# Kernel optimization log

Hardware: AMD Instinct MI355X
Metric: run time of the kernel (lower is better)

Reference implementation:

```python
import jax, jax.numpy as jnp
import numpy as np

DEPTH = 4
DIM = 768
HEADS = 12
DH = 64
INNER = HEADS * DH            # 768
FF_INNER = int(4 * (2.0 / 3.0) * DIM)  # 2048 (GEGLU paper sizing)
B, N = 4, 1024                # N must be a perfect square (2D rotary)
ATTN_SCALE = 8.0              # cosine-sim attention scale from Attention(scale=8)
EPS = 1e-5


def _ln(x, gamma, beta):
    mu = jnp.mean(x, axis=-1, keepdims=True)
    var = jnp.mean((x - mu) ** 2, axis=-1, keepdims=True)
    return (x - mu) * jax.lax.rsqrt(var + EPS) * gamma + beta


def _rope_angles(n, dh):
    # precompute_freqs_cis_2d: x/y positions on sqrt(n) grid, dh//4 freqs each, interleaved
    H = int(n ** 0.5)
    pos = jnp.arange(n)
    xp = (pos % H).astype(jnp.float32)
    yp = (pos // H).astype(jnp.float32)
    freqs = 1.0 / (10000.0 ** (jnp.arange(0, dh, 4)[: dh // 4].astype(jnp.float32) / dh))
    xa = jnp.outer(xp, freqs)  # [n, dh//4]
    ya = jnp.outer(yp, freqs)
    return jnp.stack([xa, ya], axis=-1).reshape(n, dh // 2)  # [n, dh//2]


def _apply_rope(t, cos, sin):
    # t: [B, N, H, DH]; complex-pair rotation on last dim
    tr = t.reshape(*t.shape[:-1], DH // 2, 2)
    r, im = tr[..., 0], tr[..., 1]
    c = cos[None, :, None, :]
    s = sin[None, :, None, :]
    out = jnp.stack([r * c - im * s, r * s + im * c], axis=-1)
    return out.reshape(t.shape)


def _l2norm(t):
    return t / jnp.maximum(jnp.linalg.norm(t, axis=-1, keepdims=True), 1e-12)


def setup_inputs() -> dict:
    key = jax.random.key(0)
    ks = jax.random.split(key, 10)
    w = 0.02
    return {
        "x": jax.random.normal(ks[0], (B, N, DIM), dtype=jnp.float32),
        "attn_gamma": jnp.ones((DEPTH, DIM), dtype=jnp.float32),
        "wq": w * jax.random.normal(ks[1], (DEPTH, DIM, INNER), dtype=jnp.float32),
        "wkv": w * jax.random.normal(ks[2], (DEPTH, DIM, 2 * INNER), dtype=jnp.float32),
        "q_scale": jnp.ones((DEPTH, DH), dtype=jnp.float32),
        "k_scale": jnp.ones((DEPTH, DH), dtype=jnp.float32),
        "wo": w * jax.random.normal(ks[3], (DEPTH, INNER, DIM), dtype=jnp.float32),
        "ff_gamma": jnp.ones((DEPTH, DIM), dtype=jnp.float32),
        "ff_beta": jnp.zeros((DEPTH, DIM), dtype=jnp.float32),
        "wff1": w * jax.random.normal(ks[4], (DEPTH, DIM, 2 * FF_INNER), dtype=jnp.float32),
        "wff2": w * jax.random.normal(ks[5], (DEPTH, FF_INNER, DIM), dtype=jnp.float32),
    }


def reference(x, attn_gamma, wq, wkv, q_scale, k_scale, wo, ff_gamma, ff_beta, wff1, wff2):
    b, n, _ = x.shape
    ang = _rope_angles(n, DH)
    cos, sin = jnp.cos(ang), jnp.sin(ang)
    for i in range(DEPTH):
        # ---- Attention (qk-l2norm cosine attention, 2D rotary, scale=8) ----
        h = _ln(x, attn_gamma[i], 0.0)          # Attention.norm (beta is a zero buffer)
        kv_in = x                                # faithful: kv_input taken BEFORE norm
        q = (h @ wq[i]).reshape(b, n, HEADS, DH)
        kv = kv_in @ wkv[i]
        k, v = jnp.split(kv, 2, axis=-1)
        k = k.reshape(b, n, HEADS, DH)
        v = v.reshape(b, n, HEADS, DH)
        q = _apply_rope(q, cos, sin)
        k = _apply_rope(k, cos, sin)
        q = jnp.transpose(q, (0, 2, 1, 3))       # b h n d
        k = jnp.transpose(k, (0, 2, 1, 3))
        v = jnp.transpose(v, (0, 2, 1, 3))
        q = _l2norm(q) * q_scale[i]
        k = _l2norm(k) * k_scale[i]
        sim = jnp.einsum('bhid,bhjd->bhij', q, k) * ATTN_SCALE
        attn = jax.nn.softmax(sim, axis=-1)
        o = jnp.einsum('bhij,bhjd->bhid', attn, v)
        o = jnp.transpose(o, (0, 2, 1, 3)).reshape(b, n, INNER)
        x = x + o @ wo[i]
        # ---- GEGLU FeedForward ----
        hf = _ln(x, ff_gamma[i], ff_beta[i])
        u = hf @ wff1[i]
        a, g = jnp.split(u, 2, axis=-1)
        x = x + (a * jax.nn.gelu(g, approximate=False)) @ wff2[i]
    return x
```

## Files before the change

### kernel.cpp

```cpp
#include <hip/hip_runtime.h>
#include <hip/hip_bf16.h>
#include <math.h>

typedef __hip_bfloat16 bf16;
typedef __bf16 bf16x8 __attribute__((ext_vector_type(8)));
typedef float f32x4 __attribute__((ext_vector_type(4)));

#define NDEPTH 4
#define DIM 768
#define HEADS 12
#define DH 64
#define INNER 768
#define FFI 2048
#define BB 4
#define NN 1024
#define ROWS (BB*NN)

__device__ __forceinline__ void async_cp16(const bf16* g, bf16* l) {
  __builtin_amdgcn_global_load_lds(
      (const __attribute__((address_space(1))) unsigned int*)g,
      (__attribute__((address_space(3))) unsigned int*)l, 16, 0, 0);
}

template<int BN, bool GELU, bool VOUT, int K, int LD>
__device__ __forceinline__ void gemm_body(
    const bf16* __restrict__ A, const bf16* __restrict__ Bt,
    bf16* __restrict__ Cb, float* __restrict__ Cf, const float* __restrict__ Rf,
    bf16* __restrict__ Vt, int M, int N, int bx, int by, bf16* As, bf16* Bs)
{
  constexpr int WN = BN / 2;
  constexpr int NT = WN / 16;
  const int tid  = threadIdx.x;
  const int lane = tid & 63, w = tid >> 6;
  const int quad = lane >> 4, l16 = lane & 15;
  const int wr = w >> 1, wc = w & 1;
  const int m0 = by * 128, n0 = bx * BN;

  f32x4 acc[4][NT] = {};

  constexpr int CHA = 128 * 8;
  constexpr int CH  = CHA + BN * 8;
  constexpr int NCH = CH / 256;
  constexpr int NTK = K / 64;

  auto stage = [&](int kk, int buf) {
    bf16* Asb = As + buf * (128*64);
    bf16* Bsb = Bs + buf * (BN*64);
    #pragma unroll
    for (int t = 0; t < NCH; ++t) {
      int c0 = w*64 + t*256;
      int ch = c0 + lane;
      if (c0 < CHA) {
        int r = ch >> 3, j = (ch & 7) ^ (r & 7);
        async_cp16(&A[(size_t)(m0 + r)*LD + kk + j*8], &Asb[(size_t)c0*8]);
      } else {
        int ch2 = ch - CHA, r = ch2 >> 3, j = (ch2 & 7) ^ (r & 7);
        async_cp16(&Bt[(size_t)(n0 + r)*LD + kk + j*8], &Bsb[(size_t)(c0 - CHA)*8]);
      }
    }
  };

  stage(0, 0);
  __syncthreads();

  #pragma unroll
  for (int t = 0; t < NTK; ++t) {
    const int buf = t & 1;
    if (t + 1 < NTK) stage((t + 1) * 64, buf ^ 1);

    const bf16* Asb = As + buf * (128*64);
    const bf16* Bsb = Bs + buf * (BN*64);

    #pragma unroll
    for (int kc = 0; kc < 2; ++kc) {
      bf16x8 bfr[NT];
      #pragma unroll
      for (int nt = 0; nt < NT; ++nt) {
        int rb = wc*WN + nt*16 + l16;
        int c  = (kc*4 + quad) ^ (rb & 7);
        bfr[nt] = *(const bf16x8*)&Bsb[rb*64 + c*8];
      }
      #pragma unroll
      for (int mt = 0; mt < 4; ++mt) {
        int ra = wr*64 + mt*16 + l16;
        int ca = (kc*4 + quad) ^ (ra & 7);
        bf16x8 af = *(const bf16x8*)&Asb[ra*64 + ca*8];
        #pragma unroll
        for (int nt = 0; nt < NT; ++nt)
          acc[mt][nt] = __builtin_amdgcn_mfma_f32_16x16x32_bf16(af, bfr[nt], acc[mt][nt], 0, 0, 0);
      }
    }
    if (t + 1 < NTK) __syncthreads();
  }

  #pragma unroll
  for (int mt = 0; mt < 4; ++mt) {
    #pragma unroll
    for (int nt = 0; nt < NT; ++nt) {
      int row = m0 + wr*64 + mt*16 + quad*4;
      int col = n0 + wc*WN + nt*16 + l16;
      if (GELU) {
        #pragma unroll
        for (int r = 0; r < 4; ++r) {
          float v = acc[mt][nt][r];
          float g = __shfl_xor(v, 1);
          if (!(lane & 1)) {
            float ge = 0.5f * g * (1.f + erff(g * 0.70710678118654752f));
            Cb[(size_t)(row + r)*(N >> 1) + (col >> 1)] = __float2bfloat16(v * ge);
          }
        }
      } else if (VOUT) {
        if (col < INNER) {
          #pragma unroll
          for (int r = 0; r < 4; ++r)
            Cb[(size_t)(row + r)*INNER + col] = __float2bfloat16(acc[mt][nt][r]);
        } else {
          int c2 = col - INNER, hh = c2 >> 6, d = c2 & 63;
          int b = row >> 10, nn = row & 1023;
          union { ushort4 u4; bf16 h4[4]; } p;
          #pragma unroll
          for (int r = 0; r < 4; ++r) p.h4[r] = __float2bfloat16(acc[mt][nt][r]);
          *(ushort4*)&Vt[(((size_t)b*HEADS + hh)*DH + d)*NN + nn] = p.u4;
        }
      } else {
        #pragma unroll
        for (int r = 0; r < 4; ++r) {
          float v = acc[mt][nt][r];
          size_t idx = (size_t)(row + r) * N + col;
          if (Rf) v += Rf[idx];
          if (Cf) Cf[idx] = v;
          if (Cb) Cb[idx] = __float2bfloat16(v);
        }
      }
    }
  }
}

template<int BN, int KH, int LD>
__global__ __launch_bounds__(256) void gemm_splitk_kernel(
    const bf16* __restrict__ A, const bf16* __restrict__ Bt,
    float* __restrict__ P, int M, int N)
{
  __shared__ __align__(16) bf16 As[2*128*64];
  __shared__ __align__(16) bf16 Bs[2*BN*64];
  const int z = blockIdx.z;
  gemm_body<BN,false,false,KH,LD>(A + (size_t)z*KH, Bt + (size_t)z*KH, nullptr,
                                  P + (size_t)z*M*N, nullptr, nullptr,
                                  M, N, blockIdx.x, blockIdx.y, As, Bs);
}

__global__ __launch_bounds__(256) void qkv_kernel(
    const bf16* __restrict__ h, const bf16* __restrict__ x16,
    const bf16* __restrict__ wqT, const bf16* __restrict__ wkvT,
    bf16* __restrict__ qb, bf16* __restrict__ kb, bf16* __restrict__ vt)
{
  __shared__ __align__(16) bf16 As[2*128*64];
  __shared__ __align__(16) bf16 Bs[2*128*64];
  if (blockIdx.z == 0)
    gemm_body<64,false,false,768,768>(h, wqT, qb, nullptr, nullptr, nullptr,
                                      ROWS, INNER, blockIdx.x, blockIdx.y, As, Bs);
  else
    gemm_body<128,false,true,768,768>(x16, wkvT, kb, nullptr, nullptr, vt,
                                      ROWS, 2*INNER, blockIdx.x, blockIdx.y, As, Bs);
}

__global__ __launch_bounds__(512) void gemm256_kernel(
    const bf16* __restrict__ A, const bf16* __restrict__ Bt,
    bf16* __restrict__ Cb, int M, int N)
{
  __shared__ __align__(16) bf16 As[2][256*64];
  __shared__ __align__(16) bf16 Bs[2][256*64];

  const int tid  = threadIdx.x;
  const int lane = tid & 63, wv = tid >> 6;
  const int quad = lane >> 4, l16 = lane & 15;
  const int wr = wv >> 2, wc = wv & 3;
  const int m0 = blockIdx.y * 256, n0 = blockIdx.x * 256;

  f32x4 acc[8][4] = {};

  auto stage = [&](int kk, int buf) {
    #pragma unroll
    for (int t = 0; t < 8; ++t) {
      int c0 = wv*64 + t*512;
      int ch = c0 + lane;
      if (c0 < 2048) {
        int r = ch >> 3, j = (ch & 7) ^ (r & 7);
        async_cp16(&A[(size_t)(m0 + r)*768 + kk + j*8], &As[buf][(size_t)c0*8]);
      } else {
        int ch2 = ch - 2048, r = ch2 >> 3, j = (ch2 & 7) ^ (r & 7);
        async_cp16(&Bt[(size_t)(n0 + r)*768 + kk + j*8], &Bs[buf][(size_t)(c0 - 2048)*8]);
      }
    }
  };

  stage(0, 0);
  __syncthreads();

  #pragma unroll
  for (int t = 0; t < 12; ++t) {
    const int buf = t & 1;
    if (t + 1 < 12) stage((t + 1) * 64, buf ^ 1);

    const bf16* Asb = &As[buf][0];
    const bf16* Bsb = &Bs[buf][0];

    #pragma unroll
    for (int kc = 0; kc < 2; ++kc) {
      bf16x8 bfr[4];
      #pragma unroll
      for (int nt = 0; nt < 4; ++nt) {
        int rb = wc*64 + nt*16 + l16;
        int c  = (kc*4 + quad) ^ (rb & 7);
        bfr[nt] = *(const bf16x8*)&Bsb[rb*64 + c*8];
      }
      #pragma unroll
      for (int mt = 0; mt < 8; ++mt) {
        int ra = wr*128 + mt*16 + l16;
        int ca = (kc*4 + quad) ^ (ra & 7);
        bf16x8 af = *(const bf16x8*)&Asb[ra*64 + ca*8];
        #pragma unroll
        for (int nt = 0; nt < 4; ++nt)
          acc[mt][nt] = __builtin_amdgcn_mfma_f32_16x16x32_bf16(af, bfr[nt], acc[mt][nt], 0, 0, 0);
      }
    }
    if (t + 1 < 12) __syncthreads();
  }

  #pragma unroll
  for (int mt = 0; mt < 8; ++mt) {
    #pragma unroll
    for (int nt = 0; nt < 4; ++nt) {
      int row = m0 + wr*128 + mt*16 + quad*4;
      int col = n0 + wc*64 + nt*16 + l16;
      #pragma unroll
      for (int r = 0; r < 4; ++r) {
        float v = acc[mt][nt][r];
        float g = __shfl_xor(v, 1);
        if (!(lane & 1)) {
          float ge = 0.5f * g * (1.f + erff(g * 0.70710678118654752f));
          Cb[(size_t)(row + r)*(N >> 1) + (col >> 1)] = __float2bfloat16(v * ge);
        }
      }
    }
  }
}

__global__ __launch_bounds__(256) void ln_kernel(
    const float* __restrict__ x, const float* __restrict__ g,
    const float* __restrict__ bta, bf16* __restrict__ out)
{
  const int row = blockIdx.x, tid = threadIdx.x;
  const size_t base = (size_t)row * DIM;
  float v[3];
  #pragma unroll
  for (int j = 0; j < 3; ++j) v[j] = x[base + tid + j*256];
  float s  = v[0] + v[1] + v[2];
  float ss = v[0]*v[0] + v[1]*v[1] + v[2]*v[2];
  #pragma unroll
  for (int off = 32; off; off >>= 1) { s += __shfl_xor(s, off); ss += __shfl_xor(ss, off); }
  __shared__ float red[8];
  int w = tid >> 6;
  if ((tid & 63) == 0) { red[w] = s; red[w + 4] = ss; }
  __syncthreads();
  s  = red[0] + red[1] + red[2] + red[3];
  ss = red[4] + red[5] + red[6] + red[7];
  float mean = s * (1.f/768.f);
  float var  = ss * (1.f/768.f) - mean*mean;
  float rstd = rsqrtf(fmaxf(var, 0.f) + 1e-5f);
  #pragma unroll
  for (int j = 0; j < 3; ++j) {
    int c = tid + j*256;
    float bv = bta ? bta[c] : 0.f;
    out[base + c] = __float2bfloat16((v[j] - mean) * rstd * g[c] + bv);
  }
}

__global__ __launch_bounds__(256) void redln_kernel(
    const float* __restrict__ P0, const float* __restrict__ P1,
    const float* __restrict__ res,
    float* __restrict__ xo32, bf16* __restrict__ xo16, float* __restrict__ outf,
    const float* __restrict__ g, const float* __restrict__ bta,
    bf16* __restrict__ lnout)
{
  const int row = blockIdx.x, tid = threadIdx.x;
  const size_t base = (size_t)row * DIM;
  float v[3];
  #pragma unroll
  for (int j = 0; j < 3; ++j) {
    size_t idx = base + tid + j*256;
    v[j] = res[idx] + P0[idx] + P1[idx];
    if (xo32) xo32[idx] = v[j];
    if (xo16) xo16[idx] = __float2bfloat16(v[j]);
    if (outf) outf[idx] = v[j];
  }
  if (!g) return;
  float s  = v[0] + v[1] + v[2];
  float ss = v[0]*v[0] + v[1]*v[1] + v[2]*v[2];
  #pragma unroll
  for (int off = 32; off; off >>= 1) { s += __shfl_xor(s, off); ss += __shfl_xor(ss, off); }
  __shared__ float red[8];
  int w = tid >> 6;
  if ((tid & 63) == 0) { red[w] = s; red[w + 4] = ss; }
  __syncthreads();
  s  = red[0] + red[1] + red[2] + red[3];
  ss = red[4] + red[5] + red[6] + red[7];
  float mean = s * (1.f/768.f);
  float var  = ss * (1.f/768.f) - mean*mean;
  float rstd = rsqrtf(fmaxf(var, 0.f) + 1e-5f);
  #pragma unroll
  for (int j = 0; j < 3; ++j) {
    int c = tid + j*256;
    float bv = bta ? bta[c] : 0.f;
    lnout[base + c] = __float2bfloat16((v[j] - mean) * rstd * g[c] + bv);
  }
}

__global__ __launch_bounds__(384) void rope_kernel(
    const bf16* __restrict__ q, const bf16* __restrict__ kb,
    const float* __restrict__ qsc, const float* __restrict__ ksc,
    bf16* __restrict__ qh, bf16* __restrict__ kh)
{
  const int bn = blockIdx.x;
  const int b = bn >> 10, n = bn & 1023;
  const int tid = threadIdx.x;
  const int h = tid >> 5, pr = tid & 31, d0 = pr*2;
  const float xp = (float)(n & 31), yp = (float)(n >> 5);
  const int t = pr >> 1;
  const float freq = powf(10000.f, -(float)t / 16.f);
  const float ang = (pr & 1) ? yp * freq : xp * freq;
  float sn, cs;
  sincosf(ang, &sn, &cs);
  const float2 qs2 = *(const float2*)&qsc[d0];
  const float2 ks2 = *(const float2*)&ksc[d0];

  union { unsigned int u; bf16 h2[2]; } qa, ka, qo, ko;
  qa.u = *(const unsigned int*)&q [(size_t)bn*INNER + h*64 + d0];
  ka.u = *(const unsigned int*)&kb[(size_t)bn*INNER + h*64 + d0];
  float qre = __bfloat162float(qa.h2[0]), qim = __bfloat162float(qa.h2[1]);
  float kre = __bfloat162float(ka.h2[0]), kim = __bfloat162float(ka.h2[1]);
  float qr = qre*cs - qim*sn, qi = qre*sn + qim*cs;
  float kr = kre*cs - kim*sn, ki = kre*sn + kim*cs;
  float q2 = qr*qr + qi*qi, k2 = kr*kr + ki*ki;
  #pragma unroll
  for (int off = 1; off < 32; off <<= 1) { q2 += __shfl_xor(q2, off); k2 += __shfl_xor(k2, off); }
  float qinv = 8.f / fmaxf(sqrtf(q2), 1e-12f);
  float kinv = 1.f / fmaxf(sqrtf(k2), 1e-12f);
  qo.h2[0] = __float2bfloat16(qr * qinv * qs2.x);
  qo.h2[1] = __float2bfloat16(qi * qinv * qs2.y);
  ko.h2[0] = __float2bfloat16(kr * kinv * ks2.x);
  ko.h2[1] = __float2bfloat16(ki * kinv * ks2.y);
  size_t oi = (((size_t)b*HEADS + h)*NN + n)*DH + d0;
  *(unsigned int*)&qh[oi] = qo.u;
  *(unsigned int*)&kh[oi] = ko.u;
}

__global__ __launch_bounds__(256) void attn_kernel(
    const bf16* __restrict__ qh, const bf16* __restrict__ kh,
    const bf16* __restrict__ vt, const float* __restrict__ qsc,
    const float* __restrict__ ksc, bf16* __restrict__ ob)
{
  __shared__ __align__(16) bf16 Qs[64*72];
  __shared__ __align__(16) bf16 Ks[64*72];
  __shared__ __align__(16) bf16 Vt[64*72];
  __shared__ __align__(16) bf16 Ps[4][16*72];

  const int tid = threadIdx.x;
  const int lane = tid & 63, w = tid >> 6;
  const int quad = lane >> 4, l16 = lane & 15;
  const int qt = blockIdx.x, bh = blockIdx.y;
  const int b = bh / HEADS, h = bh % HEADS;
  const size_t base = (size_t)bh * NN * DH;

  float mq = fabsf(qsc[lane]), mk = fabsf(ksc[lane]);
  #pragma unroll
  for (int off = 1; off < 64; off <<= 1) {
    mq = fmaxf(mq, __shfl_xor(mq, off));
    mk = fmaxf(mk, __shfl_xor(mk, off));
  }
  const float Mb = 8.f * mq * mk;

  for (int c = tid; c < 512; c += 256) {
    int r = c >> 3, j = c & 7;
    *(uint4*)&Qs[r*72 + j*8] = *(const uint4*)&qh[base + (size_t)(qt*64 + r)*64 + j*8];
  }

  f32x4 o[4] = {};
  float pl[4] = {0.f, 0.f, 0.f, 0.f};

  for (int kt0 = 0; kt0 < NN/64; ++kt0) {
    __syncthreads();
    for (int c = tid; c < 512; c += 256) {
      int r = c >> 3, j = c & 7;
      *(uint4*)&Ks[r*72 + j*8] = *(const uint4*)&kh[base + (size_t)(kt0*64 + r)*64 + j*8];
      *(uint4*)&Vt[r*72 + j*8] = *(const uint4*)&vt[base + (size_t)r*NN + kt0*64 + j*8];
    }
    __syncthreads();

    f32x4 s[4] = {};
    bf16x8 aq[2];
    #pragma unroll
    for (int kc = 0; kc < 2; ++kc)
      aq[kc] = *(const bf16x8*)&Qs[(w*16 + l16)*72 + kc*32 + quad*8];
    #pragma unroll
    for (int kt = 0; kt < 4; ++kt)
      #pragma unroll
      for (int kc = 0; kc < 2; ++kc) {
        bf16x8 bk = *(const bf16x8*)&Ks[(kt*16 + l16)*72 + kc*32 + quad*8];
        s[kt] = __builtin_amdgcn_mfma_f32_16x16x32_bf16(aq[kc], bk, s[kt], 0, 0, 0);
      }

    #pragma unroll
    for (int r = 0; r < 4; ++r) {
      #pragma unroll
      for (int kt = 0; kt < 4; ++kt) {
        float pv = __expf(s[kt][r] - Mb);
        pl[r] += pv;
        Ps[w][(quad*4 + r)*72 + kt*16 + l16] = __float2bfloat16(pv);
      }
    }

    #pragma unroll
    for (int kc = 0; kc < 2; ++kc) {
      bf16x8 ap = *(const bf16x8*)&Ps[w][l16*72 + kc*32 + quad*8];
      #pragma unroll
      for (int nt = 0; nt < 4; ++nt) {
        bf16x8 bv = *(const bf16x8*)&Vt[(nt*16 + l16)*72 + kc*32 + quad*8];
        o[nt] = __builtin_amdgcn_mfma_f32_16x16x32_bf16(ap, bv, o[nt], 0, 0, 0);
      }
    }
  }

  float l[4];
  #pragma unroll
  for (int r = 0; r < 4; ++r) {
    float rs = pl[r];
    #pragma unroll
    for (int off = 1; off < 16; off <<= 1) rs += __shfl_xor(rs, off);
    l[r] = rs;
  }

  #pragma unroll
  for (int nt = 0; nt < 4; ++nt)
    #pragma unroll
    for (int r = 0; r < 4; ++r) {
      int n = qt*64 + w*16 + quad*4 + r;
      int dcol = nt*16 + l16;
      ob[((size_t)(b*NN + n)*HEADS + h)*DH + dcol] = __float2bfloat16(o[nt][r] / l[r]);
    }
}

__global__ __launch_bounds__(256) void cast_kernel(
    const float* __restrict__ x, bf16* __restrict__ o)
{
  size_t i = ((size_t)blockIdx.x*256 + threadIdx.x) * 8;
  float4 f0 = *(const float4*)(x + i);
  float4 f1 = *(const float4*)(x + i + 4);
  union { uint4 u; bf16 h[8]; } p;
  p.h[0] = __float2bfloat16(f0.x); p.h[1] = __float2bfloat16(f0.y);
  p.h[2] = __float2bfloat16(f0.z); p.h[3] = __float2bfloat16(f0.w);
  p.h[4] = __float2bfloat16(f1.x); p.h[5] = __float2bfloat16(f1.y);
  p.h[6] = __float2bfloat16(f1.z); p.h[7] = __float2bfloat16(f1.w);
  *(uint4*)(o + i) = p.u;
}

struct TD { const float* src; bf16* dst; int R, C, base, perm; };
struct TDs5 { TD d[5]; };

__global__ __launch_bounds__(256) void wtrans_kernel(TDs5 a)
{
  const int blk = blockIdx.x;
  int di = 0;
  #pragma unroll
  for (int k = 1; k < 5; ++k) if (blk >= a.d[k].base) di = k;
  const TD d = a.d[di];
  const int local = blk - d.base;
  const int tilesX = d.C >> 5;
  const int by = local / tilesX, bx = local - by*tilesX;
  __shared__ float t[32][33];
  const int tx = threadIdx.x & 31, ty = threadIdx.x >> 5;
  const int c0 = bx*32, r0 = by*32;
  #pragma unroll
  for (int i = 0; i < 4; ++i)
    t[ty + i*8][tx] = d.src[(size_t)(r0 + ty + i*8)*d.C + c0 + tx];
  __syncthreads();
  const int half = d.C >> 1;
  #pragma unroll
  for (int i = 0; i < 4; ++i) {
    int c = c0 + ty + i*8;
    int rout = d.perm ? ((c < half) ? 2*c : 2*(c - half) + 1) : c;
    d.dst[(size_t)rout*d.R + r0 + tx] = __float2bfloat16(t[tx][ty + i*8]);
  }
}

extern "C" void kernel_launch(void* const* d_in, const int* in_sizes, int n_in,
                              void* d_out, int out_size, void* d_ws, size_t ws_size,
                              hipStream_t stream)
{
  const float* x_in       = (const float*)d_in[0];
  const float* attn_gamma = (const float*)d_in[1];
  const float* wq         = (const float*)d_in[2];
  const float* wkv        = (const float*)d_in[3];
  const float* q_scale    = (const float*)d_in[4];
  const float* k_scale    = (const float*)d_in[5];
  const float* wo         = (const float*)d_in[6];
  const float* ff_gamma   = (const float*)d_in[7];
  const float* ff_beta    = (const float*)d_in[8];
  const float* wff1       = (const float*)d_in[9];
  const float* wff2       = (const float*)d_in[10];
  float* outp = (float*)d_out;
  char* ws = (char*)d_ws;

  const size_t E = (size_t)ROWS * DIM;
  float* xw32 = (float*)ws;
  bf16*  xw16 = (bf16*)(ws + 12582912);
  bf16*  S_h  = (bf16*)(ws + 18874368);
  char*  BIGb = ws + 25165824;
  bf16*  WT   = (bf16*)(ws + 62914560);
  bf16*  qbuf  = (bf16*)BIGb;
  bf16*  kbuf  = qbuf + E;
  bf16*  qhb   = qbuf + 2*E;
  bf16*  khb   = qbuf + 3*E;
  bf16*  vtb   = qbuf + 4*E;
  bf16*  glbuf = (bf16*)BIGb;
  float* wP    = (float*)BIGb;
  float* fP    = (float*)(BIGb + 16777216);
  bf16*  wqT   = WT;
  bf16*  wkvT  = WT + 589824;
  bf16*  woT   = WT + 1769472;
  bf16*  wff1T = WT + 2359296;
  bf16*  wff2T = WT + 5505024;

  cast_kernel<<<1536, 256, 0, stream>>>(x_in, xw16);
  ln_kernel<<<ROWS, 256, 0, stream>>>(x_in, attn_gamma, nullptr, S_h);

  for (int i = 0; i < NDEPTH; ++i) {
    const float* xsrc = (i == 0) ? x_in : xw32;

    TDs5 td;
    td.d[0] = { wq   + (size_t)i*589824,  wqT,   768,  768,    0, 0 };
    td.d[1] = { wkv  + (size_t)i*1179648, wkvT,  768, 1536,  576, 0 };
    td.d[2] = { wo   + (size_t)i*589824,  woT,   768,  768, 1728, 0 };
    td.d[3] = { wff1 + (size_t)i*3145728, wff1T, 768, 4096, 2304, 1 };
    td.d[4] = { wff2 + (size_t)i*1572864, wff2T, 2048, 768, 5376, 0 };
    wtrans_kernel<<<6912, 256, 0, stream>>>(td);

    qkv_kernel<<<dim3(12,32,2), 256, 0, stream>>>(S_h, xw16, wqT, wkvT, qbuf, kbuf, vtb);
    rope_kernel<<<ROWS, 384, 0, stream>>>(qbuf, kbuf, q_scale + i*DH, k_scale + i*DH, qhb, khb);
    attn_kernel<<<dim3(16,48), 256, 0, stream>>>(qhb, khb, vtb,
                                                 q_scale + i*DH, k_scale + i*DH, S_h);
    gemm_splitk_kernel<64,384,768><<<dim3(12,32,2), 256, 0, stream>>>(S_h, woT, wP, ROWS, DIM);
    redln_kernel<<<ROWS, 256, 0, stream>>>(wP, wP + E, xsrc, xw32, nullptr, nullptr,
                                           ff_gamma + i*DIM, ff_beta + i*DIM, S_h);
    gemm256_kernel<<<dim3(16,16), 512, 0, stream>>>(S_h, wff1T, glbuf, ROWS, 2*FFI);
    gemm_splitk_kernel<64,1024,2048><<<dim3(12,32,2), 256, 0, stream>>>(glbuf, wff2T, fP, ROWS, DIM);
    if (i < NDEPTH-1)
      redln_kernel<<<ROWS, 256, 0, stream>>>(fP, fP + E, xw32, xw32, xw16, nullptr,
                                             attn_gamma + (i+1)*DIM, nullptr, S_h);
    else
      redln_kernel<<<ROWS, 256, 0, stream>>>(fP, fP + E, xw32, nullptr, nullptr, outp,
                                             nullptr, nullptr, nullptr);
  }
}
```

Baseline: 936.8 us.

## Double-buffer attention K/V tiles with async LDS loads and remap GEMM256 blocks per XCD

The attention kernel now loads Q, K and V with asynchronous global-to-LDS copies into XOR-swizzled, unpadded shared-memory tiles. K/V are double-buffered so the next tile's load overlaps the current tile's MFMA and softmax work, and one barrier per iteration is removed. Separately, the 256x256 GEMM remaps its linear block index so that blocks landing on the same XCD cover neighbouring tiles, to improve L2 reuse. The remap hardcodes a 16x16 grid shape, and the async loads rely on the barrier to wait for outstanding copies.

```diff
diff --git a/kernel.cpp b/kernel.cpp
--- a/kernel.cpp
+++ b/kernel.cpp
@@ -175,7 +175,12 @@
   const int lane = tid & 63, wv = tid >> 6;
   const int quad = lane >> 4, l16 = lane & 15;
   const int wr = wv >> 2, wc = wv & 3;
-  const int m0 = blockIdx.y * 256, n0 = blockIdx.x * 256;
+
+  const int lin = blockIdx.y * gridDim.x + blockIdx.x;
+  const int xcd = lin & 7, loc = lin >> 3;
+  const int bxs = (xcd & 1) * 8 + (loc & 7);
+  const int bys = (xcd >> 1) * 4 + (loc >> 3);
+  const int m0 = bys * 256, n0 = bxs * 256;
 
   f32x4 acc[8][4] = {};
 
@@ -360,9 +365,9 @@
     const bf16* __restrict__ vt, const float* __restrict__ qsc,
     const float* __restrict__ ksc, bf16* __restrict__ ob)
 {
-  __shared__ __align__(16) bf16 Qs[64*72];
-  __shared__ __align__(16) bf16 Ks[64*72];
-  __shared__ __align__(16) bf16 Vt[64*72];
+  __shared__ __align__(16) bf16 Qs[64*64];
+  __shared__ __align__(16) bf16 Ks[2][64*64];
+  __shared__ __align__(16) bf16 Vs[2][64*64];
   __shared__ __align__(16) bf16 Ps[4][16*72];
 
   const int tid = threadIdx.x;
@@ -380,33 +385,51 @@
   }
   const float Mb = 8.f * mq * mk;
 
-  for (int c = tid; c < 512; c += 256) {
-    int r = c >> 3, j = c & 7;
-    *(uint4*)&Qs[r*72 + j*8] = *(const uint4*)&qh[base + (size_t)(qt*64 + r)*64 + j*8];
-  }
+  #pragma unroll
+  for (int t = 0; t < 2; ++t) {
+    int c0 = w*64 + t*256, ch = c0 + lane;
+    int r = ch >> 3, jl = (ch & 7) ^ (r & 7);
+    async_cp16(&qh[base + (size_t)(qt*64 + r)*64 + jl*8], &Qs[(size_t)c0*8]);
+  }
+
+  auto stage_kv = [&](int kt0, int buf) {
+    #pragma unroll
+    for (int t = 0; t < 4; ++t) {
+      int c0 = w*64 + t*256, ch = c0 + lane;
+      if (c0 < 512) {
+        int r = ch >> 3, jl = (ch & 7) ^ (r & 7);
+        async_cp16(&kh[base + (size_t)(kt0*64 + r)*64 + jl*8],
+                   &Ks[buf][(size_t)c0*8]);
+      } else {
+        int ch2 = ch - 512, r = ch2 >> 3, jl = (ch2 & 7) ^ (r & 7);
+        async_cp16(&vt[base + (size_t)r*NN + kt0*64 + jl*8],
+                   &Vs[buf][(size_t)(c0 - 512)*8]);
+      }
+    }
+  };
 
   f32x4 o[4] = {};
   float pl[4] = {0.f, 0.f, 0.f, 0.f};
 
+  stage_kv(0, 0);
+  __syncthreads();
+
   for (int kt0 = 0; kt0 < NN/64; ++kt0) {
-    __syncthreads();
-    for (int c = tid; c < 512; c += 256) {
-      int r = c >> 3, j = c & 7;
-      *(uint4*)&Ks[r*72 + j*8] = *(const uint4*)&kh[base + (size_t)(kt0*64 + r)*64 + j*8];
-      *(uint4*)&Vt[r*72 + j*8] = *(const uint4*)&vt[base + (size_t)r*NN + kt0*64 + j*8];
-    }
-    __syncthreads();
+    const int buf = kt0 & 1;
+    if (kt0 + 1 < NN/64) stage_kv(kt0 + 1, buf ^ 1);
 
     f32x4 s[4] = {};
     bf16x8 aq[2];
+    const int rq = w*16 + l16;
     #pragma unroll
     for (int kc = 0; kc < 2; ++kc)
-      aq[kc] = *(const bf16x8*)&Qs[(w*16 + l16)*72 + kc*32 + quad*8];
+      aq[kc] = *(const bf16x8*)&Qs[rq*64 + ((kc*4 + quad) ^ (rq & 7))*8];
     #pragma unroll
     for (int kt = 0; kt < 4; ++kt)
       #pragma unroll
       for (int kc = 0; kc < 2; ++kc) {
-        bf16x8 bk = *(const bf16x8*)&Ks[(kt*16 + l16)*72 + kc*32 + quad*8];
+        int rb = kt*16 + l16;
+        bf16x8 bk = *(const bf16x8*)&Ks[buf][rb*64 + ((kc*4 + quad) ^ (rb & 7))*8];
         s[kt] = __builtin_amdgcn_mfma_f32_16x16x32_bf16(aq[kc], bk, s[kt], 0, 0, 0);
       }
 
@@ -425,10 +448,13 @@
       bf16x8 ap = *(const bf16x8*)&Ps[w][l16*72 + kc*32 + quad*8];
       #pragma unroll
       for (int nt = 0; nt < 4; ++nt) {
-        bf16x8 bv = *(const bf16x8*)&Vt[(nt*16 + l16)*72 + kc*32 + quad*8];
+        int rv = nt*16 + l16;
+        bf16x8 bv = *(const bf16x8*)&Vs[buf][rv*64 + ((kc*4 + quad) ^ (rv & 7))*8];
         o[nt] = __builtin_amdgcn_mfma_f32_16x16x32_bf16(ap, bv, o[nt], 0, 0, 0);
       }
     }
+
+    if (kt0 + 1 < NN/64) __syncthreads();
   }
 
   float l[4];
```

Measured after the change: 907.9 us. 3.1% less time.
